# Kernel optimization log

Measured on AMD Instinct MI355X. Metric: run time of the kernel, lower is better.

The kernel has to match this reference:

```python
import jax, jax.numpy as jnp
import numpy as np

NUM_PEAK = 28000
NUM_GENE = 12000
N_NODES = NUM_PEAK + NUM_GENE
N_EDGES = 640000
NUM_TOPICS = 100
T_HIDDEN = 512
EMB = 64
HID = 128  # 2 * emb_size, hidden_channels of GCN
BATCH = 256
BN_EPS = 1e-5


def setup_inputs() -> dict:
    key = jax.random.key(0)
    ks = iter(jax.random.split(key, 64))
    def nrm(shape, s=0.05):
        return jax.random.normal(next(ks), shape, dtype=jnp.float32) * s
    def unif(shape):
        return jax.random.uniform(next(ks), shape, dtype=jnp.float32)
    z = lambda *s: jnp.zeros(s, jnp.float32)
    o = lambda *s: jnp.ones(s, jnp.float32)
    inp = dict(
        Gene=unif((BATCH, NUM_GENE)),
        Gene_normalized=unif((BATCH, NUM_GENE)),
        Peak=unif((BATCH, NUM_PEAK)),
        Peak_normalized=unif((BATCH, NUM_PEAK)),
        feature_matrix=nrm((N_NODES, EMB), 1.0),
        # GATv2 layer 1 (EMB -> HID, heads=1)
        Wl1=nrm((HID, EMB)), bl1=z(HID), Wr1=nrm((HID, EMB)), br1=z(HID),
        att1=nrm((HID,), 0.1), bias1=z(HID),
        # GATv2 layer 2 (HID -> EMB)
        Wl2=nrm((EMB, HID)), bl2=z(EMB), Wr2=nrm((EMB, HID)), br2=z(EMB),
        att2=nrm((EMB,), 0.1), bias2=z(EMB),
        # gene encoder: Linear + ReLU + BN + Linear + ReLU + BN
        gW1=nrm((T_HIDDEN, NUM_GENE)), gb1=z(T_HIDDEN), gg1=o(T_HIDDEN), gbe1=z(T_HIDDEN),
        gW2=nrm((T_HIDDEN, T_HIDDEN)), gb2=z(T_HIDDEN), gg2=o(T_HIDDEN), gbe2=z(T_HIDDEN),
        # peak encoder
        pW1=nrm((T_HIDDEN, NUM_PEAK)), pb1=z(T_HIDDEN), pg1=o(T_HIDDEN), pbe1=z(T_HIDDEN),
        pW2=nrm((T_HIDDEN, T_HIDDEN)), pb2=z(T_HIDDEN), pg2=o(T_HIDDEN), pbe2=z(T_HIDDEN),
        mu_W=nrm((NUM_TOPICS, T_HIDDEN)), mu_b=z(NUM_TOPICS),
        ls_W=nrm((NUM_TOPICS, T_HIDDEN)), ls_b=z(NUM_TOPICS),
        alphas_W=nrm((NUM_TOPICS, EMB)),
        alphas_star_W=nrm((NUM_TOPICS, EMB)),
        edge_index=jax.random.randint(next(ks), (2, N_EDGES), 0, N_NODES),
    )
    return inp


def _batchnorm(h, gamma, beta):
    # training-style BN over batch axis (biased variance), eps=1e-5
    m = h.mean(axis=0)
    v = jnp.mean((h - m) ** 2, axis=0)
    return (h - m) * jax.lax.rsqrt(v + BN_EPS) * gamma + beta


def _gatv2(x, src, dst, Wl, bl, Wr, br, att, bias):
    # PyG GATv2Conv, heads=1: e_ij = att . leaky_relu(Wl x_j + Wr x_i),
    # softmax over incoming edges of i, out_i = sum_j alpha_ij * (Wl x_j) + bias
    xl = x @ Wl.T + bl            # [N, C]
    xr = x @ Wr.T + br            # [N, C]
    e = jax.nn.leaky_relu(xl[src] + xr[dst], negative_slope=0.2)  # [E, C]
    logit = e @ att               # [E]
    m = jax.ops.segment_max(logit, dst, num_segments=N_NODES)
    ex = jnp.exp(logit - m[dst])
    den = jax.ops.segment_sum(ex, dst, num_segments=N_NODES)
    alpha = ex / (den[dst] + 1e-16)
    out = jax.ops.segment_sum(alpha[:, None] * xl[src], dst, num_segments=N_NODES)
    return out + bias


def _encode(x, W1, b1, g1, be1, W2, b2, g2, be2, mu_W, mu_b, ls_W, ls_b):
    h = _batchnorm(jax.nn.relu(x @ W1.T + b1), g1, be1)
    h = _batchnorm(jax.nn.relu(h @ W2.T + b2), g2, be2)
    mu = h @ mu_W.T + mu_b
    logsigma = 2.0 * (h @ ls_W.T + ls_b)
    kl = -0.5 * jnp.sum(1.0 + logsigma - mu ** 2 - jnp.exp(logsigma), axis=-1).mean()
    return mu, kl


def reference(Gene, Gene_normalized, Peak, Peak_normalized, feature_matrix,
              Wl1, bl1, Wr1, br1, att1, bias1,
              Wl2, bl2, Wr2, br2, att2, bias2,
              gW1, gb1, gg1, gbe1, gW2, gb2, gg2, gbe2,
              pW1, pb1, pg1, pbe1, pW2, pb2, pg2, pbe2,
              mu_W, mu_b, ls_W, ls_b, alphas_W, alphas_star_W, edge_index):
    # ---- variational encoders (eval mode: dropout off, theta from mu) ----
    mu_d, kl_d = _encode(Gene_normalized, gW1, gb1, gg1, gbe1, gW2, gb2, gg2, gbe2,
                         mu_W, mu_b, ls_W, ls_b)
    mu_j, kl_j = _encode(Peak_normalized, pW1, pb1, pg1, pbe1, pW2, pb2, pg2, pbe2,
                         mu_W, mu_b, ls_W, ls_b)
    theta_d = jax.nn.softmax(mu_d, axis=-1)   # [B, K]
    theta_j = jax.nn.softmax(mu_j, axis=-1)
    kld_theta = kl_d + kl_j

    # ---- GCN embedding: two GATv2Conv layers with self-loops ----
    loops = jnp.arange(N_NODES)
    src = jnp.concatenate([edge_index[0], loops])
    dst = jnp.concatenate([edge_index[1], loops])
    h = jax.nn.relu(_gatv2(feature_matrix, src, dst, Wl1, bl1, Wr1, br1, att1, bias1))
    emb = _gatv2(h, src, dst, Wl2, bl2, Wr2, br2, att2, bias2)
    emb = jax.nn.relu(emb)  # theta_act applied in forward
    eta_matrix = emb[:NUM_PEAK]   # [num_peak, EMB]
    rho_matrix = emb[NUM_PEAK:]   # [num_gene, EMB]

    # ---- topic-word matrices: softmax over genes/peaks (dim=0), transposed ----
    beta_gene = jax.nn.softmax(rho_matrix @ alphas_W.T, axis=0).T        # [K, num_gene]
    beta_peak = jax.nn.softmax(eta_matrix @ alphas_star_W.T, axis=0).T   # [K, num_peak]

    # ---- decode + reconstruction loss ----
    preds_gene = jnp.log(theta_d @ beta_gene + 1e-6)
    preds_peak = jnp.log(theta_j @ beta_peak + 1e-6)
    recon = (-(preds_gene * Gene).sum(-1) - (preds_peak * Peak).sum(-1)).mean()
    return recon, kld_theta
```

## Files before the change

### kernel.cpp

```cpp
#include <hip/hip_runtime.h>
#include <cstdint>
#include <cstddef>

using u16 = unsigned short;
using u32 = unsigned int;
typedef __attribute__((ext_vector_type(8))) short bf16x8;
typedef __attribute__((ext_vector_type(4))) float f32x4;

static constexpr int NUM_PEAK = 28000;
static constexpr int NUM_GENE = 12000;
static constexpr int N_NODES  = NUM_PEAK + NUM_GENE;
static constexpr int N_EDGES  = 640000;
static constexpr int E_TOTAL  = N_EDGES + N_NODES;
static constexpr int NT       = 100;
static constexpr int NT2      = 200;
static constexpr int NTP      = 128;
static constexpr int TH       = 512;
static constexpr int EMB      = 64;
static constexpr int HID      = 128;
static constexpr int BATCH    = 256;
static constexpr int SCAN_CHUNK = 1024;
static constexpr int SCAN_NB  = (N_NODES + SCAN_CHUNK - 1) / SCAN_CHUNK;
static constexpr int ENC_CH   = 640;
static constexpr int KPG      = 12032;
static constexpr int KPP      = 28032;
static constexpr int KSPG     = (NUM_GENE + ENC_CH - 1) / ENC_CH;
static constexpr int KSPP     = (NUM_PEAK + ENC_CH - 1) / ENC_CH;
static constexpr int CS_ROWS  = 128;
static constexpr int NBMAX    = (NUM_PEAK + CS_ROWS - 1) / CS_ROWS;
#define BN_EPS 1e-5f

__device__ __forceinline__ u16 f2bf(float f) {
  u32 b = __float_as_uint(f);
  return (u16)((b + 0x7FFFu + ((b >> 16) & 1u)) >> 16);
}
__device__ __forceinline__ float bf2f(u16 u) {
  return __uint_as_float((u32)u << 16);
}

struct CvtJobs {
  const float* src[12];
  u16* dst[12];
  u32 n[12];
  u32 start[12];
  int count;
};

__global__ __launch_bounds__(256) void cvt_all(CvtJobs J) {
  const int bid = blockIdx.x;
  int seg = 0;
  while (seg + 1 < J.count && bid >= (int)J.start[seg + 1]) ++seg;
  const float* __restrict__ src = J.src[seg];
  u16* __restrict__ dst = J.dst[seg];
  const u32 n = J.n[seg];
  const u32 i = (u32)(bid - J.start[seg]) * 2048u + threadIdx.x * 8u;
  if (i + 8 <= n) {
    float4 a = *(const float4*)(src + i);
    float4 b = *(const float4*)(src + i + 4);
    ushort4 o0{f2bf(a.x), f2bf(a.y), f2bf(a.z), f2bf(a.w)};
    ushort4 o1{f2bf(b.x), f2bf(b.y), f2bf(b.z), f2bf(b.w)};
    *(ushort4*)(dst + i) = o0;
    *(ushort4*)(dst + i + 4) = o1;
  } else {
    for (u32 j = i; j < n; ++j) dst[j] = f2bf(src[j]);
  }
}

__global__ __launch_bounds__(256) void cvt_pad(
    const float* __restrict__ g, u16* __restrict__ gb,
    const float* __restrict__ p, u16* __restrict__ pb) {
  const bool sec = (blockIdx.y != 0);
  const float* __restrict__ src = sec ? p : g;
  u16* __restrict__ dst = sec ? pb : gb;
  const int K = sec ? NUM_PEAK : NUM_GENE;
  const int Kp = sec ? KPP : KPG;
  const size_t total = (size_t)BATCH * Kp;
  size_t i = ((size_t)blockIdx.x * 256 + threadIdx.x) * 8;
  const size_t stride = (size_t)gridDim.x * 256 * 8;
  for (; i < total; i += stride) {
    const int col = (int)(i % Kp);
    const size_t row = i / Kp;
    ushort4 o0{0, 0, 0, 0}, o1{0, 0, 0, 0};
    if (col + 8 <= K) {
      const float* s = src + row * K + col;
      float4 a = *(const float4*)s;
      float4 b = *(const float4*)(s + 4);
      o0 = ushort4{f2bf(a.x), f2bf(a.y), f2bf(a.z), f2bf(a.w)};
      o1 = ushort4{f2bf(b.x), f2bf(b.y), f2bf(b.z), f2bf(b.w)};
    }
    *(ushort4*)(dst + i) = o0;
    *(ushort4*)(dst + i + 4) = o1;
  }
}

struct GP {
  const u16* A; const u16* B; float* C; u16* Cb; const float* bias;
  int M, N, K, chunk;
};

__global__ __launch_bounds__(256) void gemm_bt_bf16(GP g0, GP g1, int dual) {
  const GP& g = (dual && blockIdx.z) ? g1 : g0;
  const int M = g.M, N = g.N, K = g.K;
  __shared__ u16 As[64][40];
  __shared__ u16 Bs[64][40];
  const int tid = threadIdx.x;
  const int bm = blockIdx.y * 64, bn = blockIdx.x * 64;
  if (bm >= M || bn >= N) return;
  const int k0 = dual ? 0 : blockIdx.z * g.chunk;
  const int k1 = min(K, k0 + g.chunk);
  const int w = tid >> 6, lane = tid & 63;
  const int wm = (w >> 1) * 32, wn = (w & 1) * 32;
  const int fr = lane & 15;
  const int ks = (lane >> 4) * 8;
  const int srow = tid >> 2, sseg = (tid & 3) * 8;
  f32x4 acc[2][2] = {};
  for (int kt = k0; kt < k1; kt += 32) {
    const int gk = kt + sseg;
    {
      const int gm = bm + srow;
      bf16x8 v = {0, 0, 0, 0, 0, 0, 0, 0};
      if (gm < M) {
        if (gk + 8 <= k1) v = *(const bf16x8*)(g.A + (size_t)gm * K + gk);
        else if (gk < k1)
          for (int e = 0; e < k1 - gk; ++e) ((short*)&v)[e] = (short)g.A[(size_t)gm * K + gk + e];
      }
      *(bf16x8*)&As[srow][sseg] = v;
    }
    {
      const int gn = bn + srow;
      bf16x8 v = {0, 0, 0, 0, 0, 0, 0, 0};
      if (gn < N) {
        if (gk + 8 <= k1) v = *(const bf16x8*)(g.B + (size_t)gn * K + gk);
        else if (gk < k1)
          for (int e = 0; e < k1 - gk; ++e) ((short*)&v)[e] = (short)g.B[(size_t)gn * K + gk + e];
      }
      *(bf16x8*)&Bs[srow][sseg] = v;
    }
    __syncthreads();
    bf16x8 a0 = *(const bf16x8*)&As[wm + fr][ks];
    bf16x8 a1 = *(const bf16x8*)&As[wm + 16 + fr][ks];
    bf16x8 b0 = *(const bf16x8*)&Bs[wn + fr][ks];
    bf16x8 b1 = *(const bf16x8*)&Bs[wn + 16 + fr][ks];
    acc[0][0] = __builtin_amdgcn_mfma_f32_16x16x32_bf16(a0, b0, acc[0][0], 0, 0, 0);
    acc[0][1] = __builtin_amdgcn_mfma_f32_16x16x32_bf16(a0, b1, acc[0][1], 0, 0, 0);
    acc[1][0] = __builtin_amdgcn_mfma_f32_16x16x32_bf16(a1, b0, acc[1][0], 0, 0, 0);
    acc[1][1] = __builtin_amdgcn_mfma_f32_16x16x32_bf16(a1, b1, acc[1][1], 0, 0, 0);
    __syncthreads();
  }
  const bool split = (!dual && gridDim.z > 1);
#pragma unroll
  for (int fi = 0; fi < 2; ++fi)
#pragma unroll
    for (int fj = 0; fj < 2; ++fj)
#pragma unroll
      for (int r = 0; r < 4; ++r) {
        const int row = bm + wm + fi * 16 + (lane >> 4) * 4 + r;
        const int col = bn + wn + fj * 16 + fr;
        if (row < M && col < N) {
          const float v = acc[fi][fj][r];
          if (split) atomicAdd(&g.C[(size_t)row * N + col], v);
          else if (g.Cb) g.Cb[(size_t)row * N + col] = f2bf(v + (g.bias ? g.bias[col] : 0.f));
          else g.C[(size_t)row * N + col] = v + (g.bias ? g.bias[col] : 0.f);
        }
      }
}

__device__ __forceinline__ int swz64(int row, int colu16) {
  return row * 64 + ((((colu16 >> 3) ^ row) & 7) << 3) + (colu16 & 7);
}

__global__ __launch_bounds__(256) void gemm_enc1(
    const u16* __restrict__ A0, const float* __restrict__ B0, float* __restrict__ P0,
    int K0, int Kp0, int ksp0,
    const u16* __restrict__ A1, const float* __restrict__ B1, float* __restrict__ P1,
    int K1, int Kp1) {
  int bx = blockIdx.x, by = blockIdx.y, bz = blockIdx.z;
  {
    const int gx = gridDim.x, gy = gridDim.y;
    const int nwg = gx * gy * gridDim.z;
    if ((nwg & 7) == 0) {
      const int f = bx + gx * (by + gy * bz);
      const int cpx = nwg >> 3;
      const int f2 = (f & 7) * cpx + (f >> 3);
      bx = f2 % gx;
      by = (f2 / gx) % gy;
      bz = f2 / (gx * gy);
    }
  }
  const bool second = (bz >= ksp0);
  const u16* __restrict__ A = second ? A1 : A0;
  const float* __restrict__ B = second ? B1 : B0;
  float* __restrict__ P = second ? P1 : P0;
  const int K = second ? K1 : K0;
  const int Kp = second ? Kp1 : Kp0;
  const int zz = second ? bz - ksp0 : bz;
  const int k0 = zz * ENC_CH;
  const int k1 = min(K, k0 + ENC_CH);
  __shared__ u16 As[64 * 64];
  __shared__ u16 Bs[64 * 64];
  const int tid = threadIdx.x;
  const int bm = by * 64;
  const int bn = bx * 64;
  const int w = tid >> 6, lane = tid & 63;
  const int wm = w * 16;
  const int fr = lane & 15, g = lane >> 4;
  const int ar = tid >> 2, acol = (tid & 3) * 16;
  const int br = tid >> 2, bcol = (tid & 3) * 16;
  const u16* Abase = A + (size_t)(bm + ar) * Kp + acol;
  const float* Bbase = B + (size_t)(bn + br) * K + bcol;

  bf16x8 rA0, rA1;
  float4 rB0, rB1, rB2, rB3;
  auto LD = [&](int kt) {
    const u16* sa = Abase + kt;
    rA0 = *(const bf16x8*)(sa);
    rA1 = *(const bf16x8*)(sa + 8);
    if (kt + bcol + 16 <= K) {
      const float* sb = Bbase + kt;
      rB0 = *(const float4*)(sb);
      rB1 = *(const float4*)(sb + 4);
      rB2 = *(const float4*)(sb + 8);
      rB3 = *(const float4*)(sb + 12);
    } else {
      rB0 = float4{0.f, 0.f, 0.f, 0.f}; rB1 = rB0; rB2 = rB0; rB3 = rB0;
    }
  };
  auto ST = [&]() {
    *(bf16x8*)&As[swz64(ar, acol)] = rA0;
    *(bf16x8*)&As[swz64(ar, acol + 8)] = rA1;
    ushort4 p0{f2bf(rB0.x), f2bf(rB0.y), f2bf(rB0.z), f2bf(rB0.w)};
    ushort4 p1{f2bf(rB1.x), f2bf(rB1.y), f2bf(rB1.z), f2bf(rB1.w)};
    ushort4 p2{f2bf(rB2.x), f2bf(rB2.y), f2bf(rB2.z), f2bf(rB2.w)};
    ushort4 p3{f2bf(rB3.x), f2bf(rB3.y), f2bf(rB3.z), f2bf(rB3.w)};
    const int b0 = swz64(br, bcol);
    const int b1 = swz64(br, bcol + 8);
    *(ushort4*)&Bs[b0] = p0;
    *(ushort4*)&Bs[b0 + 4] = p1;
    *(ushort4*)&Bs[b1] = p2;
    *(ushort4*)&Bs[b1 + 4] = p3;
  };

  f32x4 acc[4] = {};
  LD(k0);
  ST();
  for (int kt = k0; kt < k1; kt += 64) {
    __syncthreads();
    const bool more = (kt + 64 < k1);
    if (more) LD(kt + 64);
#pragma unroll
    for (int s = 0; s < 2; ++s) {
      const int kc = s * 32 + g * 8;
      bf16x8 a = *(const bf16x8*)&As[swz64(wm + fr, kc)];
#pragma unroll
      for (int fj = 0; fj < 4; ++fj) {
        bf16x8 b = *(const bf16x8*)&Bs[swz64(fj * 16 + fr, kc)];
        acc[fj] = __builtin_amdgcn_mfma_f32_16x16x32_bf16(a, b, acc[fj], 0, 0, 0);
      }
    }
    __syncthreads();
    if (more) ST();
  }
  float* Pz = P + (size_t)zz * TH * 256;
  const int row = bm + wm + g * 4;
#pragma unroll
  for (int fj = 0; fj < 4; ++fj) {
    const int col = bn + fj * 16 + fr;
    *(f32x4*)&Pz[(size_t)col * 256 + row] = acc[fj];
  }
}

__global__ __launch_bounds__(256) void bias_relu_bn_part(
    const float* __restrict__ PG, int nzG, const float* __restrict__ bg,
    const float* __restrict__ gg, const float* __restrict__ beg,
    u16* __restrict__ og,
    const float* __restrict__ PP, int nzP, const float* __restrict__ bp,
    const float* __restrict__ gp, const float* __restrict__ bep,
    u16* __restrict__ op) {
  int c = blockIdx.x;
  const float *P, *b, *gma, *be; u16* ob; int nz;
  if (c < TH) { P = PG; nz = nzG; b = bg; gma = gg; be = beg; ob = og; }
  else { c -= TH; P = PP; nz = nzP; b = bp; gma = gp; be = bep; ob = op; }
  const int r = threadIdx.x;
  float v = 0.f;
  const float* base = P + (size_t)c * 256 + r;
  for (int z = 0; z < nz; ++z) v += base[(size_t)z * TH * 256];
  v = fmaxf(v + b[c], 0.f);
  __shared__ float red[BATCH];
  red[r] = v; __syncthreads();
  for (int s = BATCH / 2; s > 0; s >>= 1) { if (r < s) red[r] += red[r + s]; __syncthreads(); }
  const float mean = red[0] * (1.f / BATCH);
  __syncthreads();
  const float d = v - mean;
  red[r] = d * d; __syncthreads();
  for (int s = BATCH / 2; s > 0; s >>= 1) { if (r < s) red[r] += red[r + s]; __syncthreads(); }
  const float var = red[0] * (1.f / BATCH);
  ob[(size_t)r * TH + c] = f2bf(d * rsqrtf(var + BN_EPS) * gma[c] + be[c]);
}

__global__ __launch_bounds__(256) void recon_fused(
    const u16* __restrict__ thg, const u16* __restrict__ betag,
    const float* __restrict__ Xg, int Ng, int tiles_g,
    const u16* __restrict__ thp, const u16* __restrict__ betap,
    const float* __restrict__ Xp, int Np, float* __restrict__ partials) {
  __shared__ float pred[64][65];
  __shared__ float wsum[4];
  int ct = blockIdx.x;
  const u16* A; const u16* B; const float* X; int N;
  if (ct < tiles_g) { A = thg; B = betag; X = Xg; N = Ng; }
  else { ct -= tiles_g; A = thp; B = betap; X = Xp; N = Np; }
  const int bm = blockIdx.y * 64, bn = ct * 64;
  const int tid = threadIdx.x, w = tid >> 6, lane = tid & 63;
  const int wm = (w >> 1) * 32, wn = (w & 1) * 32;
  const int fr = lane & 15, ks = (lane >> 4) * 8;
  const u16* Ar0 = A + (size_t)(bm + wm + fr) * NTP;
  const u16* Ar1 = A + (size_t)(bm + wm + 16 + fr) * NTP;
  bf16x8 a0[4], a1[4];
#pragma unroll
  for (int kt = 0; kt < 4; ++kt) {
    a0[kt] = *(const bf16x8*)(Ar0 + kt * 32 + ks);
    a1[kt] = *(const bf16x8*)(Ar1 + kt * 32 + ks);
  }
  const int gn0 = min(bn + wn + fr, N - 1);
  const int gn1 = min(bn + wn + 16 + fr, N - 1);
  const u16* Br0 = B + (size_t)gn0 * NTP;
  const u16* Br1 = B + (size_t)gn1 * NTP;
  f32x4 acc[2][2] = {};
#pragma unroll
  for (int kt = 0; kt < 4; ++kt) {
    bf16x8 b0 = *(const bf16x8*)(Br0 + kt * 32 + ks);
    bf16x8 b1 = *(const bf16x8*)(Br1 + kt * 32 + ks);
    acc[0][0] = __builtin_amdgcn_mfma_f32_16x16x32_bf16(a0[kt], b0, acc[0][0], 0, 0, 0);
    acc[0][1] = __builtin_amdgcn_mfma_f32_16x16x32_bf16(a0[kt], b1, acc[0][1], 0, 0, 0);
    acc[1][0] = __builtin_amdgcn_mfma_f32_16x16x32_bf16(a1[kt], b0, acc[1][0], 0, 0, 0);
    acc[1][1] = __builtin_amdgcn_mfma_f32_16x16x32_bf16(a1[kt], b1, acc[1][1], 0, 0, 0);
  }
#pragma unroll
  for (int fi = 0; fi < 2; ++fi)
#pragma unroll
    for (int fj = 0; fj < 2; ++fj)
#pragma unroll
      for (int r = 0; r < 4; ++r)
        pred[wm + fi * 16 + (lane >> 4) * 4 + r][wn + fj * 16 + fr] = acc[fi][fj][r];
  __syncthreads();
  float local = 0.f;
  if (bn + 64 <= N) {
#pragma unroll
    for (int k = 0; k < 4; ++k) {
      const int j = k * 1024 + tid * 4;
      const int row = j >> 6, col = j & 63;
      const float4 xv = *(const float4*)(X + (size_t)(bm + row) * N + bn + col);
      local += xv.x * __logf(pred[row][col + 0] + 1e-6f);
      local += xv.y * __logf(pred[row][col + 1] + 1e-6f);
      local += xv.z * __logf(pred[row][col + 2] + 1e-6f);
      local += xv.w * __logf(pred[row][col + 3] + 1e-6f);
    }
  } else {
#pragma unroll
    for (int k = 0; k < 16; ++k) {
      const int idx = k * 256 + tid, row = idx >> 6, col = idx & 63;
      if (bn + col < N)
        local += X[(size_t)(bm + row) * N + bn + col] * __logf(pred[row][col] + 1e-6f);
    }
  }
  for (int o = 32; o > 0; o >>= 1) local += __shfl_down(local, o);
  if (lane == 0) wsum[w] = local;
  __syncthreads();
  if (tid == 0)
    partials[(size_t)blockIdx.y * gridDim.x + blockIdx.x] =
        wsum[0] + wsum[1] + wsum[2] + wsum[3];
}

__global__ __launch_bounds__(256) void final_recon(
    const float* __restrict__ partials, int n, float* __restrict__ out) {
  float s = 0.f;
  for (int i = threadIdx.x; i < n; i += 256) s += partials[i];
  __shared__ float red[256];
  red[threadIdx.x] = s; __syncthreads();
  for (int o = 128; o > 0; o >>= 1) {
    if (threadIdx.x < o) red[threadIdx.x] += red[threadIdx.x + o];
    __syncthreads();
  }
  if (threadIdx.x == 0) out[0] = -red[0] * (1.f / BATCH);
}

__global__ __launch_bounds__(256) void bias_relu_bn2(
    const float* __restrict__ Hg, const float* __restrict__ bg,
    const float* __restrict__ gg, const float* __restrict__ beg,
    u16* __restrict__ og,
    const float* __restrict__ Hp, const float* __restrict__ bp,
    const float* __restrict__ gp, const float* __restrict__ bep,
    u16* __restrict__ op) {
  int c = blockIdx.x;
  const float *H, *b, *gma, *be; u16* ob;
  if (c < TH) { H = Hg; b = bg; gma = gg; be = beg; ob = og; }
  else { c -= TH; H = Hp; b = bp; gma = gp; be = bep; ob = op; }
  const int r = threadIdx.x;
  float v = fmaxf(H[(size_t)r * TH + c] + b[c], 0.f);
  __shared__ float red[BATCH];
  red[r] = v; __syncthreads();
  for (int s = BATCH / 2; s > 0; s >>= 1) { if (r < s) red[r] += red[r + s]; __syncthreads(); }
  const float mean = red[0] * (1.f / BATCH);
  __syncthreads();
  const float d = v - mean;
  red[r] = d * d; __syncthreads();
  for (int s = BATCH / 2; s > 0; s >>= 1) { if (r < s) red[r] += red[r + s]; __syncthreads(); }
  const float var = red[0] * (1.f / BATCH);
  ob[(size_t)r * TH + c] = f2bf(d * rsqrtf(var + BN_EPS) * gma[c] + be[c]);
}

__global__ __launch_bounds__(128) void row_kl_theta(
    const float* __restrict__ mld, const float* __restrict__ mlj,
    const float* __restrict__ mu_b, const float* __restrict__ ls_b,
    u16* __restrict__ thd, u16* __restrict__ thj, float* __restrict__ kl_out) {
  const float* ml = blockIdx.y ? mlj : mld;
  u16* thb = blockIdx.y ? thj : thd;
  const int b = blockIdx.x;
  const int t = threadIdx.x;
  const bool act = (t < NT);
  float mu = 0.f, ls = 0.f, term = 0.f;
  if (act) {
    mu = ml[(size_t)b * NT2 + t] + mu_b[t];
    ls = 2.f * (ml[(size_t)b * NT2 + NT + t] + ls_b[t]);
    term = 1.f + ls - mu * mu - expf(ls);
  }
  __shared__ float red[128];
  red[t] = act ? term : 0.f; __syncthreads();
  for (int s = 64; s > 0; s >>= 1) { if (t < s) red[t] += red[t + s]; __syncthreads(); }
  if (t == 0) atomicAdd(kl_out, -0.5f * red[0] * (1.f / BATCH));
  __syncthreads();
  red[t] = act ? mu : -INFINITY; __syncthreads();
  for (int s = 64; s > 0; s >>= 1) { if (t < s) red[t] = fmaxf(red[t], red[t + s]); __syncthreads(); }
  const float mx = red[0];
  __syncthreads();
  const float e = act ? expf(mu - mx) : 0.f;
  red[t] = e; __syncthreads();
  for (int s = 64; s > 0; s >>= 1) { if (t < s) red[t] += red[t + s]; __syncthreads(); }
  thb[(size_t)b * NTP + t] = act ? f2bf(e / red[0]) : (u16)0;
}

__global__ __launch_bounds__(256) void deg_count(
    const int* __restrict__ ei, int* __restrict__ deg) {
  int e = blockIdx.x * 256 + threadIdx.x;
  if (e >= E_TOTAL) return;
  const int d = (e < N_EDGES) ? ei[N_EDGES + e] : e - N_EDGES;
  atomicAdd(&deg[d], 1);
}

__global__ __launch_bounds__(256) void scan_part(
    const int* __restrict__ deg, int* __restrict__ bsum) {
  const int base = blockIdx.x * SCAN_CHUNK + threadIdx.x * 4;
  int s = 0;
#pragma unroll
  for (int i = 0; i < 4; ++i) {
    const int idx = base + i;
    if (idx < N_NODES) s += deg[idx];
  }
  for (int o = 32; o > 0; o >>= 1) s += __shfl_down(s, o);
  __shared__ int ws[4];
  if ((threadIdx.x & 63) == 0) ws[threadIdx.x >> 6] = s;
  __syncthreads();
  if (threadIdx.x == 0) bsum[blockIdx.x] = ws[0] + ws[1] + ws[2] + ws[3];
}

__global__ __launch_bounds__(64) void scan_bsum(int* __restrict__ bsum) {
  if (threadIdx.x == 0) {
    int run = 0;
    for (int i = 0; i < SCAN_NB; ++i) { int v = bsum[i]; bsum[i] = run; run += v; }
  }
}

__global__ __launch_bounds__(256) void scan_final(
    const int* __restrict__ deg, const int* __restrict__ bsum,
    int* __restrict__ row_ptr) {
  const int t = threadIdx.x;
  const int base = blockIdx.x * SCAN_CHUNK + t * 4;
  int v[4], s = 0;
#pragma unroll
  for (int i = 0; i < 4; ++i) {
    const int idx = base + i;
    v[i] = (idx < N_NODES) ? deg[idx] : 0;
    s += v[i];
  }
  const int lane = t & 63, w = t >> 6;
  int x = s;
  for (int o = 1; o < 64; o <<= 1) {
    int y = __shfl_up(x, o);
    if (lane >= o) x += y;
  }
  __shared__ int wtot[4];
  if (lane == 63) wtot[w] = x;
  __syncthreads();
  int woff = 0;
  for (int i = 0; i < w; ++i) woff += wtot[i];
  int excl = bsum[blockIdx.x] + woff + x - s;
#pragma unroll
  for (int i = 0; i < 4; ++i) {
    const int idx = base + i;
    if (idx < N_NODES) { row_ptr[idx] = excl; excl += v[i]; }
  }
  if (blockIdx.x == 0 && t == 0) row_ptr[N_NODES] = E_TOTAL;
}

__global__ __launch_bounds__(256) void csr_scatter(
    const int* __restrict__ ei, const int* __restrict__ row_ptr,
    int* __restrict__ cur, int* __restrict__ csr_src) {
  int e = blockIdx.x * 256 + threadIdx.x;
  if (e >= E_TOTAL) return;
  int s, d;
  if (e < N_EDGES) { s = ei[e]; d = ei[N_EDGES + e]; }
  else { s = d = e - N_EDGES; }
  const int pos = atomicAdd(&cur[d], 1);
  csr_src[row_ptr[d] + pos] = s;
}

template <int C>
__global__ __launch_bounds__(256) void gat_fused(
    const u16* __restrict__ xl, const u16* __restrict__ xr,
    const float* __restrict__ att, const float* __restrict__ bias,
    const int* __restrict__ row_ptr, const int* __restrict__ csr_src,
    u16* __restrict__ out_b) {
  constexpr int CPL = C / 8;
  constexpr int W = CPL / 2;
  const int lane = threadIdx.x & 63;
  const int g = lane >> 3, li = lane & 7;
  const int d = blockIdx.x * 4 + (threadIdx.x >> 6);
  if (d >= N_NODES) return;
  const int c0 = li * CPL;
  float xrv[CPL], attv[CPL], acc[CPL];
  {
    const u32* xrw = (const u32*)(xr + (size_t)d * C + c0);
#pragma unroll
    for (int i = 0; i < W; ++i) {
      const u32 wv = xrw[i];
      xrv[2 * i]     = __uint_as_float(wv << 16);
      xrv[2 * i + 1] = __uint_as_float(wv & 0xffff0000u);
    }
  }
#pragma unroll
  for (int i = 0; i < CPL; ++i) { attv[i] = att[c0 + i]; acc[i] = 0.f; }
  float m = -INFINITY, den = 0.f;
  const int end = row_ptr[d + 1];
  int p = row_ptr[d] + g;
  int s = (p < end) ? csr_src[p] : 0;
  u32 w[W];
  {
    const u32* sw = (const u32*)(xl + (size_t)s * C + c0);
#pragma unroll
    for (int i = 0; i < W; ++i) w[i] = sw[i];
  }
  while (p < end) {
    const int sn = (p + 8 < end) ? csr_src[p + 8] : 0;
    u32 wn[W];
    {
      const u32* sw = (const u32*)(xl + (size_t)sn * C + c0);
#pragma unroll
      for (int i = 0; i < W; ++i) wn[i] = sw[i];
    }
    float xlv[CPL];
#pragma unroll
    for (int i = 0; i < W; ++i) {
      xlv[2 * i]     = __uint_as_float(w[i] << 16);
      xlv[2 * i + 1] = __uint_as_float(w[i] & 0xffff0000u);
    }
    float part = 0.f;
#pragma unroll
    for (int i = 0; i < CPL; ++i) {
      float x = xlv[i] + xrv[i];
      x = (x > 0.f) ? x : 0.2f * x;
      part += x * attv[i];
    }
    part += __shfl_xor(part, 1);
    part += __shfl_xor(part, 2);
    part += __shfl_xor(part, 4);
    const float nm = fmaxf(m, part);
    const float scale = __expf(m - nm);
    const float ex = __expf(part - nm);
    den = den * scale + ex;
#pragma unroll
    for (int i = 0; i < CPL; ++i) acc[i] = acc[i] * scale + ex * xlv[i];
    m = nm;
    p += 8;
#pragma unroll
    for (int i = 0; i < W; ++i) w[i] = wn[i];
  }
  float M = m;
  M = fmaxf(M, __shfl_xor(M, 8));
  M = fmaxf(M, __shfl_xor(M, 16));
  M = fmaxf(M, __shfl_xor(M, 32));
  const float gs = __expf(m - M);
  den *= gs;
  den += __shfl_xor(den, 8);
  den += __shfl_xor(den, 16);
  den += __shfl_xor(den, 32);
  const float inv = 1.f / (den + 1e-16f);
  float va[CPL];
#pragma unroll
  for (int i = 0; i < CPL; ++i) {
    float a = acc[i] * gs;
    a += __shfl_xor(a, 8);
    a += __shfl_xor(a, 16);
    a += __shfl_xor(a, 32);
    va[i] = a;
  }
  if (g == 0) {
    u32* dst = (u32*)(out_b + (size_t)d * C + c0);
#pragma unroll
    for (int i = 0; i < W; ++i) {
      const u16 lo = f2bf(fmaxf(va[2 * i] * inv + bias[c0 + 2 * i], 0.f));
      const u16 hi = f2bf(fmaxf(va[2 * i + 1] * inv + bias[c0 + 2 * i + 1], 0.f));
      dst[i] = (u32)lo | ((u32)hi << 16);
    }
  }
}

__global__ __launch_bounds__(128) void col_stats(
    const float* __restrict__ Lg, const float* __restrict__ Lp,
    float* __restrict__ bstats) {
  const bool sec = (blockIdx.y != 0);
  const float* L = sec ? Lp : Lg;
  const int M = sec ? NUM_PEAK : NUM_GENE;
  const int r0 = blockIdx.x * CS_ROWS;
  const int c = threadIdx.x;
  if (c >= NT || r0 >= M) return;
  const int rend = min(r0 + CS_ROWS, M);
  float m = -INFINITY, s = 0.f;
  for (int r = r0; r < rend; ++r) {
    const float v = L[(size_t)r * NT + c];
    const float nm = fmaxf(m, v);
    s = s * __expf(m - nm) + __expf(v - nm);
    m = nm;
  }
  float* bs = bstats + (((size_t)blockIdx.y * NT + c) * NBMAX + blockIdx.x) * 2;
  bs[0] = m;
  bs[1] = s;
}

__global__ __launch_bounds__(64) void col_merge(
    const float* __restrict__ bstats, int nbG, int nbP,
    float* __restrict__ mstat, float* __restrict__ istat) {
  const bool sec = (blockIdx.y != 0);
  const int nb = sec ? nbP : nbG;
  const int c = blockIdx.x;
  const int l = threadIdx.x;
  const float* bs = bstats + ((size_t)blockIdx.y * NT + c) * NBMAX * 2;
  float m = -INFINITY, s = 0.f;
  for (int b = l; b < nb; b += 64) {
    const float mb = bs[b * 2];
    const float sb = bs[b * 2 + 1];
    const float nm = fmaxf(m, mb);
    s = s * __expf(m - nm) + sb * __expf(mb - nm);
    m = nm;
  }
#pragma unroll
  for (int o = 32; o > 0; o >>= 1) {
    const float mo = __shfl_xor(m, o);
    const float so = __shfl_xor(s, o);
    const float nm = fmaxf(m, mo);
    s = s * __expf(m - nm) + so * __expf(mo - nm);
    m = nm;
  }
  if (l == 0) {
    mstat[blockIdx.y * NT + c] = m;
    istat[blockIdx.y * NT + c] = 1.f / s;
  }
}

__global__ __launch_bounds__(256) void beta_norm(
    const float* __restrict__ Lg, const float* __restrict__ Lp,
    const float* __restrict__ mstat, const float* __restrict__ istat,
    u16* __restrict__ og, u16* __restrict__ op) {
  const float* L = blockIdx.y ? Lp : Lg;
  const int M = blockIdx.y ? NUM_PEAK : NUM_GENE;
  const float* mxg = mstat + blockIdx.y * NT;
  const float* ivg = istat + blockIdx.y * NT;
  u16* o = blockIdx.y ? op : og;
  __shared__ float mx[NT], inv[NT];
  for (int i = threadIdx.x; i < NT; i += 256) { mx[i] = mxg[i]; inv[i] = ivg[i]; }
  __syncthreads();
  const size_t total = (size_t)M * NTP;
  size_t i = (size_t)blockIdx.x * 256 + threadIdx.x;
  const size_t stride = (size_t)gridDim.x * 256;
  for (; i < total; i += stride) {
    const int c = (int)(i & (NTP - 1));
    u16 v = 0;
    if (c < NT) {
      const size_t r = i >> 7;
      v = f2bf(__expf(L[r * NT + c] - mx[c]) * inv[c]);
    }
    o[i] = v;
  }
}

extern "C" void kernel_launch(void* const* d_in, const int* in_sizes, int n_in,
                              void* d_out, int out_size, void* d_ws, size_t ws_size,
                              hipStream_t stream) {
  const float* Gene  = (const float*)d_in[0];
  const float* GeneN = (const float*)d_in[1];
  const float* Peak  = (const float*)d_in[2];
  const float* PeakN = (const float*)d_in[3];
  const float* feat  = (const float*)d_in[4];
  const float* Wl1 = (const float*)d_in[5];  const float* bl1 = (const float*)d_in[6];
  const float* Wr1 = (const float*)d_in[7];  const float* br1 = (const float*)d_in[8];
  const float* att1 = (const float*)d_in[9]; const float* bias1 = (const float*)d_in[10];
  const float* Wl2 = (const float*)d_in[11]; const float* bl2 = (const float*)d_in[12];
  const float* Wr2 = (const float*)d_in[13]; const float* br2 = (const float*)d_in[14];
  const float* att2 = (const float*)d_in[15]; const float* bias2 = (const float*)d_in[16];
  const float* gW1 = (const float*)d_in[17]; const float* gb1 = (const float*)d_in[18];
  const float* gg1 = (const float*)d_in[19]; const float* gbe1 = (const float*)d_in[20];
  const float* gW2 = (const float*)d_in[21]; const float* gb2 = (const float*)d_in[22];
  const float* gg2 = (const float*)d_in[23]; const float* gbe2 = (const float*)d_in[24];
  const float* pW1 = (const float*)d_in[25]; const float* pb1 = (const float*)d_in[26];
  const float* pg1 = (const float*)d_in[27]; const float* pbe1 = (const float*)d_in[28];
  const float* pW2 = (const float*)d_in[29]; const float* pb2 = (const float*)d_in[30];
  const float* pg2 = (const float*)d_in[31]; const float* pbe2 = (const float*)d_in[32];
  const float* mu_W = (const float*)d_in[33]; const float* mu_b = (const float*)d_in[34];
  const float* ls_W = (const float*)d_in[35]; const float* ls_b = (const float*)d_in[36];
  const float* alphas_W = (const float*)d_in[37];
  const float* alphas_star_W = (const float*)d_in[38];
  const int* ei = (const int*)d_in[39];
  float* out = (float*)d_out;
  (void)in_sizes; (void)n_in; (void)ws_size;

  char* base = (char*)d_ws;
  size_t off = 0;
  auto A = [&](size_t bytes) { void* p = base + off; off += (bytes + 255) & ~(size_t)255; return p; };
  int* deg     = (int*)A((size_t)N_NODES * 4);
  int* cur     = (int*)A((size_t)N_NODES * 4);
  int* row_ptr = (int*)A((size_t)(N_NODES + 1) * 4);
  int* bsum    = (int*)A((size_t)(SCAN_NB + 1) * 4);
  int* csr_src = (int*)A((size_t)E_TOTAL * 4);
  float* CpartG = (float*)A((size_t)KSPG * TH * 256 * 4);
  float* CpartP = (float*)A((size_t)KSPP * TH * 256 * 4);
  float* h2g = (float*)A((size_t)BATCH * TH * 4);
  float* h2p = (float*)A((size_t)BATCH * TH * 4);
  u16* h1gb = (u16*)A((size_t)BATCH * TH * 2);
  u16* h2gb = (u16*)A((size_t)BATCH * TH * 2);
  u16* h1pb = (u16*)A((size_t)BATCH * TH * 2);
  u16* h2pb = (u16*)A((size_t)BATCH * TH * 2);
  float* ml_d = (float*)A((size_t)BATCH * NT2 * 4);
  float* ml_j = (float*)A((size_t)BATCH * NT2 * 4);
  u16* th_db = (u16*)A((size_t)BATCH * NTP * 2);
  u16* th_jb = (u16*)A((size_t)BATCH * NTP * 2);
  float* lgg = (float*)A((size_t)NUM_GENE * NT * 4);
  float* lgp = (float*)A((size_t)NUM_PEAK * NT * 4);
  u16* betagb = (u16*)A((size_t)NUM_GENE * NTP * 2);
  u16* betapb = (u16*)A((size_t)NUM_PEAK * NTP * 2);
  u16* featb = (u16*)A((size_t)N_NODES * EMB * 2);
  u16* gW2b = (u16*)A((size_t)TH * TH * 2);
  u16* pW2b = (u16*)A((size_t)TH * TH * 2);
  u16* mlWb = (u16*)A((size_t)NT2 * TH * 2);
  u16* Wl1b = (u16*)A((size_t)HID * EMB * 2);
  u16* Wr1b = (u16*)A((size_t)HID * EMB * 2);
  u16* Wl2b = (u16*)A((size_t)EMB * HID * 2);
  u16* Wr2b = (u16*)A((size_t)EMB * HID * 2);
  u16* aWb  = (u16*)A((size_t)NT * EMB * 2);
  u16* aSWb = (u16*)A((size_t)NT * EMB * 2);
  u16* agg1b = (u16*)A((size_t)N_NODES * HID * 2);
  u16* embb  = (u16*)A((size_t)N_NODES * EMB * 2);
  float* mstat = (float*)A(2 * NT * 4);
  float* istat = (float*)A(2 * NT * 4);
  float* bstats = (float*)A((size_t)2 * NT * NBMAX * 2 * 4);
  float* partials = (float*)A(4096 * 4);
  u16* xl1b = (u16*)A((size_t)N_NODES * HID * 2);
  u16* xr1b = (u16*)A((size_t)N_NODES * HID * 2);
  u16* xl2b = (u16*)A((size_t)N_NODES * EMB * 2);
  u16* xr2b = (u16*)A((size_t)N_NODES * EMB * 2);
  u16* GeneNb = (u16*)A((size_t)BATCH * KPG * 2);
  u16* PeakNb = (u16*)A((size_t)BATCH * KPP * 2);

  auto cdiv = [](int a, int b) { return (a + b - 1) / b; };
  auto Z = [&](void* p, size_t bytes) { hipMemsetAsync(p, 0, bytes, stream); };

  Z(d_out, (size_t)out_size * sizeof(float));
  Z(deg, 2 * (size_t)N_NODES * 4);

  deg_count<<<cdiv(E_TOTAL, 256), 256, 0, stream>>>(ei, deg);
  scan_part<<<SCAN_NB, 256, 0, stream>>>(deg, bsum);
  scan_bsum<<<1, 64, 0, stream>>>(bsum);
  scan_final<<<SCAN_NB, 256, 0, stream>>>(deg, bsum, row_ptr);
  csr_scatter<<<cdiv(E_TOTAL, 256), 256, 0, stream>>>(ei, row_ptr, cur, csr_src);

  {
    const int blocks = cdiv(BATCH * KPP / 8, 256);
    cvt_pad<<<dim3(blocks, 2), 256, 0, stream>>>(GeneN, GeneNb, PeakN, PeakNb);
  }

  {
    CvtJobs J = {};
    int c = 0; u32 blocks = 0;
    auto add = [&](const float* s, u16* d, size_t n) {
      J.src[c] = s; J.dst[c] = d; J.n[c] = (u32)n; J.start[c] = blocks;
      blocks += (u32)((n + 2047) / 2048); ++c;
    };
    add(gW2, gW2b, (size_t)TH * TH);
    add(pW2, pW2b, (size_t)TH * TH);
    add(mu_W, mlWb, (size_t)NT * TH);
    add(ls_W, mlWb + (size_t)NT * TH, (size_t)NT * TH);
    add(feat, featb, (size_t)N_NODES * EMB);
    add(Wl1, Wl1b, (size_t)HID * EMB);
    add(Wr1, Wr1b, (size_t)HID * EMB);
    add(Wl2, Wl2b, (size_t)EMB * HID);
    add(Wr2, Wr2b, (size_t)EMB * HID);
    add(alphas_W, aWb, (size_t)NT * EMB);
    add(alphas_star_W, aSWb, (size_t)NT * EMB);
    J.count = c;
    cvt_all<<<blocks, 256, 0, stream>>>(J);
  }

  gemm_enc1<<<dim3(TH / 64, BATCH / 64, KSPG + KSPP), 256, 0, stream>>>(
      GeneNb, gW1, CpartG, NUM_GENE, KPG, KSPG,
      PeakNb, pW1, CpartP, NUM_PEAK, KPP);
  bias_relu_bn_part<<<2 * TH, BATCH, 0, stream>>>(
      CpartG, KSPG, gb1, gg1, gbe1, h1gb,
      CpartP, KSPP, pb1, pg1, pbe1, h1pb);
  {
    GP g = {h1gb, gW2b, h2g, nullptr, nullptr, BATCH, TH, TH, TH};
    GP p = {h1pb, pW2b, h2p, nullptr, nullptr, BATCH, TH, TH, TH};
    gemm_bt_bf16<<<dim3(TH / 64, BATCH / 64, 2), 256, 0, stream>>>(g, p, 1);
  }
  bias_relu_bn2<<<2 * TH, BATCH, 0, stream>>>(h2g, gb2, gg2, gbe2, h2gb,
                                              h2p, pb2, pg2, pbe2, h2pb);
  {
    GP g = {h2gb, mlWb, ml_d, nullptr, nullptr, BATCH, NT2, TH, TH};
    GP p = {h2pb, mlWb, ml_j, nullptr, nullptr, BATCH, NT2, TH, TH};
    gemm_bt_bf16<<<dim3(cdiv(NT2, 64), BATCH / 64, 2), 256, 0, stream>>>(g, p, 1);
  }
  row_kl_theta<<<dim3(BATCH, 2), 128, 0, stream>>>(ml_d, ml_j, mu_b, ls_b, th_db, th_jb, out + 1);

  {
    GP l = {featb, Wl1b, nullptr, xl1b, bl1, N_NODES, HID, EMB, EMB};
    GP r = {featb, Wr1b, nullptr, xr1b, br1, N_NODES, HID, EMB, EMB};
    gemm_bt_bf16<<<dim3(HID / 64, N_NODES / 64, 2), 256, 0, stream>>>(l, r, 1);
  }
  gat_fused<HID><<<N_NODES / 4, 256, 0, stream>>>(xl1b, xr1b, att1, bias1, row_ptr, csr_src, agg1b);

  {
    GP l = {agg1b, Wl2b, nullptr, xl2b, bl2, N_NODES, EMB, HID, HID};
    GP r = {agg1b, Wr2b, nullptr, xr2b, br2, N_NODES, EMB, HID, HID};
    gemm_bt_bf16<<<dim3(EMB / 64, N_NODES / 64, 2), 256, 0, stream>>>(l, r, 1);
  }
  gat_fused<EMB><<<N_NODES / 4, 256, 0, stream>>>(xl2b, xr2b, att2, bias2, row_ptr, csr_src, embb);

  {
    GP g = {embb + (size_t)NUM_PEAK * EMB, aWb, lgg, nullptr, nullptr, NUM_GENE, NT, EMB, EMB};
    GP p = {embb, aSWb, lgp, nullptr, nullptr, NUM_PEAK, NT, EMB, EMB};
    gemm_bt_bf16<<<dim3(2, cdiv(NUM_PEAK, 64), 2), 256, 0, stream>>>(g, p, 1);
  }
  const int nbG = cdiv(NUM_GENE, CS_ROWS);
  const int nbP = cdiv(NUM_PEAK, CS_ROWS);
  col_stats<<<dim3(NBMAX, 2), 128, 0, stream>>>(lgg, lgp, bstats);
  col_merge<<<dim3(NT, 2), 64, 0, stream>>>(bstats, nbG, nbP, mstat, istat);
  beta_norm<<<dim3(1024, 2), 256, 0, stream>>>(lgg, lgp, mstat, istat, betagb, betapb);

  const int tiles_g = cdiv(NUM_GENE, 64);
  const int tiles_p = cdiv(NUM_PEAK, 64);
  const int tiles = tiles_g + tiles_p;
  recon_fused<<<dim3(tiles, 4), 256, 0, stream>>>(
      th_db, betagb, Gene, NUM_GENE, tiles_g,
      th_jb, betapb, Peak, NUM_PEAK, partials);
  final_recon<<<1, 256, 0, stream>>>(partials, tiles * 4, out);
}
```

Before: 394.4 us.

## Merge independent encoder and GAT stages into combined mega-kernels by block range

Independent branches (encoder GEMMs and BN, GAT linear layers and aggregation, KL/theta and column stats) are turned into device functions and dispatched from shared launches, with each launch splitting its blocks by index range. This cuts the number of kernel launches and lets the small encoder work overlap with the large graph work instead of running serially. The GEMM helper drops split-K and tail handling, which assumes K is a multiple of 32. Shared memory is now sized for the largest branch, which may lower occupancy for the lighter ones.

```diff
diff --git a/kernel.cpp b/kernel.cpp
--- a/kernel.cpp
+++ b/kernel.cpp
@@ -26,6 +26,7 @@
 static constexpr int KPP      = 28032;
 static constexpr int KSPG     = (NUM_GENE + ENC_CH - 1) / ENC_CH;
 static constexpr int KSPP     = (NUM_PEAK + ENC_CH - 1) / ENC_CH;
+static constexpr int ENC1B    = 8 * 4 * (KSPG + KSPP);
 static constexpr int CS_ROWS  = 128;
 static constexpr int NBMAX    = (NUM_PEAK + CS_ROWS - 1) / CS_ROWS;
 #define BN_EPS 1e-5f
@@ -33,9 +34,6 @@
 __device__ __forceinline__ u16 f2bf(float f) {
   u32 b = __float_as_uint(f);
   return (u16)((b + 0x7FFFu + ((b >> 16) & 1u)) >> 16);
-}
-__device__ __forceinline__ float bf2f(u16 u) {
-  return __uint_as_float((u32)u << 16);
 }
 
 struct CvtJobs {
@@ -95,45 +93,34 @@
 
 struct GP {
   const u16* A; const u16* B; float* C; u16* Cb; const float* bias;
-  int M, N, K, chunk;
+  int M, N, K;
 };
 
-__global__ __launch_bounds__(256) void gemm_bt_bf16(GP g0, GP g1, int dual) {
-  const GP& g = (dual && blockIdx.z) ? g1 : g0;
+__device__ void dev_gemm_bt(const GP g, int bxx, int byy, char* smem) {
+  u16 (*As)[40] = (u16(*)[40])smem;
+  u16 (*Bs)[40] = (u16(*)[40])(smem + 64 * 40 * 2);
   const int M = g.M, N = g.N, K = g.K;
-  __shared__ u16 As[64][40];
-  __shared__ u16 Bs[64][40];
   const int tid = threadIdx.x;
-  const int bm = blockIdx.y * 64, bn = blockIdx.x * 64;
+  const int bm = byy * 64, bn = bxx * 64;
   if (bm >= M || bn >= N) return;
-  const int k0 = dual ? 0 : blockIdx.z * g.chunk;
-  const int k1 = min(K, k0 + g.chunk);
   const int w = tid >> 6, lane = tid & 63;
   const int wm = (w >> 1) * 32, wn = (w & 1) * 32;
   const int fr = lane & 15;
   const int ks = (lane >> 4) * 8;
   const int srow = tid >> 2, sseg = (tid & 3) * 8;
   f32x4 acc[2][2] = {};
-  for (int kt = k0; kt < k1; kt += 32) {
+  for (int kt = 0; kt < K; kt += 32) {
     const int gk = kt + sseg;
     {
       const int gm = bm + srow;
       bf16x8 v = {0, 0, 0, 0, 0, 0, 0, 0};
-      if (gm < M) {
-        if (gk + 8 <= k1) v = *(const bf16x8*)(g.A + (size_t)gm * K + gk);
-        else if (gk < k1)
-          for (int e = 0; e < k1 - gk; ++e) ((short*)&v)[e] = (short)g.A[(size_t)gm * K + gk + e];
-      }
+      if (gm < M) v = *(const bf16x8*)(g.A + (size_t)gm * K + gk);
       *(bf16x8*)&As[srow][sseg] = v;
     }
     {
       const int gn = bn + srow;
       bf16x8 v = {0, 0, 0, 0, 0, 0, 0, 0};
-      if (gn < N) {
-        if (gk + 8 <= k1) v = *(const bf16x8*)(g.B + (size_t)gn * K + gk);
-        else if (gk < k1)
-          for (int e = 0; e < k1 - gk; ++e) ((short*)&v)[e] = (short)g.B[(size_t)gn * K + gk + e];
-      }
+      if (gn < N) v = *(const bf16x8*)(g.B + (size_t)gn * K + gk);
       *(bf16x8*)&Bs[srow][sseg] = v;
     }
     __syncthreads();
@@ -147,7 +134,6 @@
     acc[1][1] = __builtin_amdgcn_mfma_f32_16x16x32_bf16(a1, b1, acc[1][1], 0, 0, 0);
     __syncthreads();
   }
-  const bool split = (!dual && gridDim.z > 1);
 #pragma unroll
   for (int fi = 0; fi < 2; ++fi)
 #pragma unroll
@@ -158,8 +144,7 @@
         const int col = bn + wn + fj * 16 + fr;
         if (row < M && col < N) {
           const float v = acc[fi][fj][r];
-          if (split) atomicAdd(&g.C[(size_t)row * N + col], v);
-          else if (g.Cb) g.Cb[(size_t)row * N + col] = f2bf(v + (g.bias ? g.bias[col] : 0.f));
+          if (g.Cb) g.Cb[(size_t)row * N + col] = f2bf(v + (g.bias ? g.bias[col] : 0.f));
           else g.C[(size_t)row * N + col] = v + (g.bias ? g.bias[col] : 0.f);
         }
       }
@@ -169,35 +154,26 @@
   return row * 64 + ((((colu16 >> 3) ^ row) & 7) << 3) + (colu16 & 7);
 }
 
-__global__ __launch_bounds__(256) void gemm_enc1(
+__device__ void dev_enc1(
     const u16* __restrict__ A0, const float* __restrict__ B0, float* __restrict__ P0,
-    int K0, int Kp0, int ksp0,
     const u16* __restrict__ A1, const float* __restrict__ B1, float* __restrict__ P1,
-    int K1, int Kp1) {
-  int bx = blockIdx.x, by = blockIdx.y, bz = blockIdx.z;
-  {
-    const int gx = gridDim.x, gy = gridDim.y;
-    const int nwg = gx * gy * gridDim.z;
-    if ((nwg & 7) == 0) {
-      const int f = bx + gx * (by + gy * bz);
-      const int cpx = nwg >> 3;
-      const int f2 = (f & 7) * cpx + (f >> 3);
-      bx = f2 % gx;
-      by = (f2 / gx) % gy;
-      bz = f2 / (gx * gy);
-    }
-  }
-  const bool second = (bz >= ksp0);
+    int bid, char* smem) {
+  const int cpx = ENC1B >> 3;
+  const int f2 = (bid & 7) * cpx + (bid >> 3);
+  const int bx = f2 % 8;
+  const int by = (f2 / 8) % 4;
+  const int bz = f2 / 32;
+  const bool second = (bz >= KSPG);
   const u16* __restrict__ A = second ? A1 : A0;
   const float* __restrict__ B = second ? B1 : B0;
   float* __restrict__ P = second ? P1 : P0;
-  const int K = second ? K1 : K0;
-  const int Kp = second ? Kp1 : Kp0;
-  const int zz = second ? bz - ksp0 : bz;
+  const int K = second ? NUM_PEAK : NUM_GENE;
+  const int Kp = second ? KPP : KPG;
+  const int zz = second ? bz - KSPG : bz;
   const int k0 = zz * ENC_CH;
   const int k1 = min(K, k0 + ENC_CH);
-  __shared__ u16 As[64 * 64];
-  __shared__ u16 Bs[64 * 64];
+  u16* As = (u16*)smem;
+  u16* Bs = (u16*)(smem + 8192);
   const int tid = threadIdx.x;
   const int bm = by * 64;
   const int bn = bx * 64;
@@ -269,23 +245,109 @@
   }
 }
 
-__global__ __launch_bounds__(256) void bias_relu_bn_part(
-    const float* __restrict__ PG, int nzG, const float* __restrict__ bg,
-    const float* __restrict__ gg, const float* __restrict__ beg,
-    u16* __restrict__ og,
-    const float* __restrict__ PP, int nzP, const float* __restrict__ bp,
-    const float* __restrict__ gp, const float* __restrict__ bep,
-    u16* __restrict__ op) {
-  int c = blockIdx.x;
-  const float *P, *b, *gma, *be; u16* ob; int nz;
-  if (c < TH) { P = PG; nz = nzG; b = bg; gma = gg; be = beg; ob = og; }
-  else { c -= TH; P = PP; nz = nzP; b = bp; gma = gp; be = bep; ob = op; }
+template <int C>
+__device__ void dev_gat(
+    const u16* __restrict__ xl, const u16* __restrict__ xr,
+    const float* __restrict__ att, const float* __restrict__ bias,
+    const int* __restrict__ row_ptr, const int* __restrict__ csr_src,
+    u16* __restrict__ out_b, int blk) {
+  constexpr int CPL = C / 8;
+  constexpr int W = CPL / 2;
+  const int lane = threadIdx.x & 63;
+  const int g = lane >> 3, li = lane & 7;
+  const int d = blk * 4 + ((int)threadIdx.x >> 6);
+  if (d >= N_NODES) return;
+  const int c0 = li * CPL;
+  float xrv[CPL], attv[CPL], acc[CPL];
+  {
+    const u32* xrw = (const u32*)(xr + (size_t)d * C + c0);
+#pragma unroll
+    for (int i = 0; i < W; ++i) {
+      const u32 wv = xrw[i];
+      xrv[2 * i]     = __uint_as_float(wv << 16);
+      xrv[2 * i + 1] = __uint_as_float(wv & 0xffff0000u);
+    }
+  }
+#pragma unroll
+  for (int i = 0; i < CPL; ++i) { attv[i] = att[c0 + i]; acc[i] = 0.f; }
+  float m = -INFINITY, den = 0.f;
+  const int end = row_ptr[d + 1];
+  int p = row_ptr[d] + g;
+  int s = (p < end) ? csr_src[p] : 0;
+  u32 w[W];
+  {
+    const u32* sw = (const u32*)(xl + (size_t)s * C + c0);
+#pragma unroll
+    for (int i = 0; i < W; ++i) w[i] = sw[i];
+  }
+  while (p < end) {
+    const int sn = (p + 8 < end) ? csr_src[p + 8] : 0;
+    u32 wn[W];
+    {
+      const u32* sw = (const u32*)(xl + (size_t)sn * C + c0);
+#pragma unroll
+      for (int i = 0; i < W; ++i) wn[i] = sw[i];
+    }
+    float xlv[CPL];
+#pragma unroll
+    for (int i = 0; i < W; ++i) {
+      xlv[2 * i]     = __uint_as_float(w[i] << 16);
+      xlv[2 * i + 1] = __uint_as_float(w[i] & 0xffff0000u);
+    }
+    float part = 0.f;
+#pragma unroll
+    for (int i = 0; i < CPL; ++i) {
+      float x = xlv[i] + xrv[i];
+      x = (x > 0.f) ? x : 0.2f * x;
+      part += x * attv[i];
+    }
+    part += __shfl_xor(part, 1);
+    part += __shfl_xor(part, 2);
+    part += __shfl_xor(part, 4);
+    const float nm = fmaxf(m, part);
+    const float scale = __expf(m - nm);
+    const float ex = __expf(part - nm);
+    den = den * scale + ex;
+#pragma unroll
+    for (int i = 0; i < CPL; ++i) acc[i] = acc[i] * scale + ex * xlv[i];
+    m = nm;
+    p += 8;
+#pragma unroll
+    for (int i = 0; i < W; ++i) w[i] = wn[i];
+  }
+  float M = m;
+  M = fmaxf(M, __shfl_xor(M, 8));
+  M = fmaxf(M, __shfl_xor(M, 16));
+  M = fmaxf(M, __shfl_xor(M, 32));
+  const float gs = __expf(m - M);
+  den *= gs;
+  den += __shfl_xor(den, 8);
+  den += __shfl_xor(den, 16);
+  den += __shfl_xor(den, 32);
+  const float inv = 1.f / (den + 1e-16f);
+  float va[CPL];
+#pragma unroll
+  for (int i = 0; i < CPL; ++i) {
+    float a = acc[i] * gs;
+    a += __shfl_xor(a, 8);
+    a += __shfl_xor(a, 16);
+    a += __shfl_xor(a, 32);
+    va[i] = a;
+  }
+  if (g == 0) {
+    u32* dst = (u32*)(out_b + (size_t)d * C + c0);
+#pragma unroll
+    for (int i = 0; i < W; ++i) {
+      const u16 lo = f2bf(fmaxf(va[2 * i] * inv + bias[c0 + 2 * i], 0.f));
+      const u16 hi = f2bf(fmaxf(va[2 * i + 1] * inv + bias[c0 + 2 * i + 1], 0.f));
+      dst[i] = (u32)lo | ((u32)hi << 16);
+    }
+  }
+}
+
+__device__ void dev_bn_body(float v, const float* gma, const float* be, int c,
+                            u16* ob, float* red) {
   const int r = threadIdx.x;
-  float v = 0.f;
-  const float* base = P + (size_t)c * 256 + r;
-  for (int z = 0; z < nz; ++z) v += base[(size_t)z * TH * 256];
-  v = fmaxf(v + b[c], 0.f);
-  __shared__ float red[BATCH];
   red[r] = v; __syncthreads();
   for (int s = BATCH / 2; s > 0; s >>= 1) { if (r < s) red[r] += red[r + s]; __syncthreads(); }
   const float mean = red[0] * (1.f / BATCH);
@@ -297,124 +359,43 @@
   ob[(size_t)r * TH + c] = f2bf(d * rsqrtf(var + BN_EPS) * gma[c] + be[c]);
 }
 
-__global__ __launch_bounds__(256) void recon_fused(
-    const u16* __restrict__ thg, const u16* __restrict__ betag,
-    const float* __restrict__ Xg, int Ng, int tiles_g,
-    const u16* __restrict__ thp, const u16* __restrict__ betap,
-    const float* __restrict__ Xp, int Np, float* __restrict__ partials) {
-  __shared__ float pred[64][65];
-  __shared__ float wsum[4];
-  int ct = blockIdx.x;
-  const u16* A; const u16* B; const float* X; int N;
-  if (ct < tiles_g) { A = thg; B = betag; X = Xg; N = Ng; }
-  else { ct -= tiles_g; A = thp; B = betap; X = Xp; N = Np; }
-  const int bm = blockIdx.y * 64, bn = ct * 64;
-  const int tid = threadIdx.x, w = tid >> 6, lane = tid & 63;
-  const int wm = (w >> 1) * 32, wn = (w & 1) * 32;
-  const int fr = lane & 15, ks = (lane >> 4) * 8;
-  const u16* Ar0 = A + (size_t)(bm + wm + fr) * NTP;
-  const u16* Ar1 = A + (size_t)(bm + wm + 16 + fr) * NTP;
-  bf16x8 a0[4], a1[4];
-#pragma unroll
-  for (int kt = 0; kt < 4; ++kt) {
-    a0[kt] = *(const bf16x8*)(Ar0 + kt * 32 + ks);
-    a1[kt] = *(const bf16x8*)(Ar1 + kt * 32 + ks);
-  }
-  const int gn0 = min(bn + wn + fr, N - 1);
-  const int gn1 = min(bn + wn + 16 + fr, N - 1);
-  const u16* Br0 = B + (size_t)gn0 * NTP;
-  const u16* Br1 = B + (size_t)gn1 * NTP;
-  f32x4 acc[2][2] = {};
-#pragma unroll
-  for (int kt = 0; kt < 4; ++kt) {
-    bf16x8 b0 = *(const bf16x8*)(Br0 + kt * 32 + ks);
-    bf16x8 b1 = *(const bf16x8*)(Br1 + kt * 32 + ks);
-    acc[0][0] = __builtin_amdgcn_mfma_f32_16x16x32_bf16(a0[kt], b0, acc[0][0], 0, 0, 0);
-    acc[0][1] = __builtin_amdgcn_mfma_f32_16x16x32_bf16(a0[kt], b1, acc[0][1], 0, 0, 0);
-    acc[1][0] = __builtin_amdgcn_mfma_f32_16x16x32_bf16(a1[kt], b0, acc[1][0], 0, 0, 0);
-    acc[1][1] = __builtin_amdgcn_mfma_f32_16x16x32_bf16(a1[kt], b1, acc[1][1], 0, 0, 0);
-  }
-#pragma unroll
-  for (int fi = 0; fi < 2; ++fi)
-#pragma unroll
-    for (int fj = 0; fj < 2; ++fj)
-#pragma unroll
-      for (int r = 0; r < 4; ++r)
-        pred[wm + fi * 16 + (lane >> 4) * 4 + r][wn + fj * 16 + fr] = acc[fi][fj][r];
-  __syncthreads();
-  float local = 0.f;
-  if (bn + 64 <= N) {
-#pragma unroll
-    for (int k = 0; k < 4; ++k) {
-      const int j = k * 1024 + tid * 4;
-      const int row = j >> 6, col = j & 63;
-      const float4 xv = *(const float4*)(X + (size_t)(bm + row) * N + bn + col);
-      local += xv.x * __logf(pred[row][col + 0] + 1e-6f);
-      local += xv.y * __logf(pred[row][col + 1] + 1e-6f);
-      local += xv.z * __logf(pred[row][col + 2] + 1e-6f);
-      local += xv.w * __logf(pred[row][col + 3] + 1e-6f);
-    }
-  } else {
-#pragma unroll
-    for (int k = 0; k < 16; ++k) {
-      const int idx = k * 256 + tid, row = idx >> 6, col = idx & 63;
-      if (bn + col < N)
-        local += X[(size_t)(bm + row) * N + bn + col] * __logf(pred[row][col] + 1e-6f);
-    }
-  }
-  for (int o = 32; o > 0; o >>= 1) local += __shfl_down(local, o);
-  if (lane == 0) wsum[w] = local;
-  __syncthreads();
-  if (tid == 0)
-    partials[(size_t)blockIdx.y * gridDim.x + blockIdx.x] =
-        wsum[0] + wsum[1] + wsum[2] + wsum[3];
-}
-
-__global__ __launch_bounds__(256) void final_recon(
-    const float* __restrict__ partials, int n, float* __restrict__ out) {
-  float s = 0.f;
-  for (int i = threadIdx.x; i < n; i += 256) s += partials[i];
-  __shared__ float red[256];
-  red[threadIdx.x] = s; __syncthreads();
-  for (int o = 128; o > 0; o >>= 1) {
-    if (threadIdx.x < o) red[threadIdx.x] += red[threadIdx.x + o];
-    __syncthreads();
-  }
-  if (threadIdx.x == 0) out[0] = -red[0] * (1.f / BATCH);
-}
-
-__global__ __launch_bounds__(256) void bias_relu_bn2(
-    const float* __restrict__ Hg, const float* __restrict__ bg,
-    const float* __restrict__ gg, const float* __restrict__ beg,
-    u16* __restrict__ og,
-    const float* __restrict__ Hp, const float* __restrict__ bp,
-    const float* __restrict__ gp, const float* __restrict__ bep,
-    u16* __restrict__ op) {
-  int c = blockIdx.x;
+__device__ void dev_bn_part(
+    int cg, const float* __restrict__ PG, int nzG, const float* bg,
+    const float* gg, const float* beg, u16* og,
+    const float* __restrict__ PP, int nzP, const float* bp,
+    const float* gp, const float* bep, u16* op, float* red) {
+  int c = cg;
+  const float *P, *b, *gma, *be; u16* ob; int nz;
+  if (c < TH) { P = PG; nz = nzG; b = bg; gma = gg; be = beg; ob = og; }
+  else { c -= TH; P = PP; nz = nzP; b = bp; gma = gp; be = bep; ob = op; }
+  const int r = threadIdx.x;
+  float v = 0.f;
+  const float* base = P + (size_t)c * 256 + r;
+  for (int z = 0; z < nz; ++z) v += base[(size_t)z * TH * 256];
+  v = fmaxf(v + b[c], 0.f);
+  dev_bn_body(v, gma, be, c, ob, red);
+}
+
+__device__ void dev_bn2(
+    int cg, const float* __restrict__ Hg, const float* bg,
+    const float* gg, const float* beg, u16* og,
+    const float* __restrict__ Hp, const float* bp,
+    const float* gp, const float* bep, u16* op, float* red) {
+  int c = cg;
   const float *H, *b, *gma, *be; u16* ob;
   if (c < TH) { H = Hg; b = bg; gma = gg; be = beg; ob = og; }
   else { c -= TH; H = Hp; b = bp; gma = gp; be = bep; ob = op; }
   const int r = threadIdx.x;
   float v = fmaxf(H[(size_t)r * TH + c] + b[c], 0.f);
-  __shared__ float red[BATCH];
-  red[r] = v; __syncthreads();
-  for (int s = BATCH / 2; s > 0; s >>= 1) { if (r < s) red[r] += red[r + s]; __syncthreads(); }
-  const float mean = red[0] * (1.f / BATCH);
-  __syncthreads();
-  const float d = v - mean;
-  red[r] = d * d; __syncthreads();
-  for (int s = BATCH / 2; s > 0; s >>= 1) { if (r < s) red[r] += red[r + s]; __syncthreads(); }
-  const float var = red[0] * (1.f / BATCH);
-  ob[(size_t)r * TH + c] = f2bf(d * rsqrtf(var + BN_EPS) * gma[c] + be[c]);
-}
-
-__global__ __launch_bounds__(128) void row_kl_theta(
-    const float* __restrict__ mld, const float* __restrict__ mlj,
-    const float* __restrict__ mu_b, const float* __restrict__ ls_b,
-    u16* __restrict__ thd, u16* __restrict__ thj, float* __restrict__ kl_out) {
-  const float* ml = blockIdx.y ? mlj : mld;
-  u16* thb = blockIdx.y ? thj : thd;
-  const int b = blockIdx.x;
+  dev_bn_body(v, gma, be, c, ob, red);
+}
+
+__device__ void dev_row_kl(
+    int b, int which, const float* __restrict__ mld, const float* __restrict__ mlj,
+    const float* mu_b, const float* ls_b,
+    u16* thd, u16* thj, float* kl_out, float* red) {
+  const float* ml = which ? mlj : mld;
+  u16* thb = which ? thj : thd;
   const int t = threadIdx.x;
   const bool act = (t < NT);
   float mu = 0.f, ls = 0.f, term = 0.f;
@@ -423,7 +404,6 @@
     ls = 2.f * (ml[(size_t)b * NT2 + NT + t] + ls_b[t]);
     term = 1.f + ls - mu * mu - expf(ls);
   }
-  __shared__ float red[128];
   red[t] = act ? term : 0.f; __syncthreads();
   for (int s = 64; s > 0; s >>= 1) { if (t < s) red[t] += red[t + s]; __syncthreads(); }
   if (t == 0) atomicAdd(kl_out, -0.5f * red[0] * (1.f / BATCH));
@@ -438,6 +418,110 @@
   thb[(size_t)b * NTP + t] = act ? f2bf(e / red[0]) : (u16)0;
 }
 
+__device__ void dev_col_stats(
+    int bx, int sec, const float* __restrict__ Lg, const float* __restrict__ Lp,
+    float* __restrict__ bstats) {
+  const float* L = sec ? Lp : Lg;
+  const int M = sec ? NUM_PEAK : NUM_GENE;
+  const int r0 = bx * CS_ROWS;
+  const int c = threadIdx.x;
+  if (c >= NT || r0 >= M) return;
+  const int rend = min(r0 + CS_ROWS, M);
+  float m = -INFINITY, s = 0.f;
+  for (int r = r0; r < rend; ++r) {
+    const float v = L[(size_t)r * NT + c];
+    const float nm = fmaxf(m, v);
+    s = s * __expf(m - nm) + __expf(v - nm);
+    m = nm;
+  }
+  float* bs = bstats + (((size_t)sec * NT + c) * NBMAX + bx) * 2;
+  bs[0] = m;
+  bs[1] = s;
+}
+
+__global__ __launch_bounds__(256) void mega1(
+    const u16* A0, const float* B0, float* P0,
+    const u16* A1, const float* B1, float* P1,
+    GP l, GP r) {
+  __shared__ __align__(16) char smem[20480];
+  const int bid = blockIdx.x;
+  if (bid < ENC1B) {
+    dev_enc1(A0, B0, P0, A1, B1, P1, bid, smem);
+  } else {
+    const int sub = bid - ENC1B;
+    const GP& g = (sub >= 1250) ? r : l;
+    const int rem = sub % 1250;
+    dev_gemm_bt(g, rem % 2, rem / 2, smem);
+  }
+}
+
+__global__ __launch_bounds__(256) void mega2(
+    const float* PG, int nzG, const float* bg, const float* gg, const float* beg, u16* og,
+    const float* PP, int nzP, const float* bp, const float* gp, const float* bep, u16* op,
+    const u16* xl, const u16* xr, const float* att, const float* bias,
+    const int* row_ptr, const int* csr_src, u16* out_b) {
+  __shared__ float red[256];
+  const int bid = blockIdx.x;
+  if (bid < 2 * TH)
+    dev_bn_part(bid, PG, nzG, bg, gg, beg, og, PP, nzP, bp, gp, bep, op, red);
+  else
+    dev_gat<HID>(xl, xr, att, bias, row_ptr, csr_src, out_b, bid - 2 * TH);
+}
+
+__global__ __launch_bounds__(256) void mega3(GP eg, GP ep, GP l, GP r) {
+  __shared__ __align__(16) char smem[20480];
+  const int bid = blockIdx.x;
+  if (bid < 64) {
+    const int z = bid >> 5, rem = bid & 31;
+    dev_gemm_bt(z ? ep : eg, rem & 7, rem >> 3, smem);
+  } else {
+    const int sub = bid - 64;
+    const GP& g = (sub >= 625) ? r : l;
+    dev_gemm_bt(g, 0, sub % 625, smem);
+  }
+}
+
+__global__ __launch_bounds__(256) void mega4(
+    const float* Hg, const float* bg, const float* gg, const float* beg, u16* og,
+    const float* Hp, const float* bp, const float* gp, const float* bep, u16* op,
+    const u16* xl, const u16* xr, const float* att, const float* bias,
+    const int* row_ptr, const int* csr_src, u16* out_b) {
+  __shared__ float red[256];
+  const int bid = blockIdx.x;
+  if (bid < 2 * TH)
+    dev_bn2(bid, Hg, bg, gg, beg, og, Hp, bp, gp, bep, op, red);
+  else
+    dev_gat<EMB>(xl, xr, att, bias, row_ptr, csr_src, out_b, bid - 2 * TH);
+}
+
+__global__ __launch_bounds__(256) void mega5(GP hg, GP hp, GP tg, GP tp) {
+  __shared__ __align__(16) char smem[20480];
+  const int bid = blockIdx.x;
+  if (bid < 32) {
+    const int z = bid >> 4, rem = bid & 15;
+    dev_gemm_bt(z ? hp : hg, rem & 3, rem >> 2, smem);
+  } else {
+    const int sub = bid - 32;
+    const GP& g = (sub >= 876) ? tp : tg;
+    const int rem = sub % 876;
+    dev_gemm_bt(g, rem & 1, rem >> 1, smem);
+  }
+}
+
+__global__ __launch_bounds__(128) void mega6(
+    const float* mld, const float* mlj, const float* mu_b, const float* ls_b,
+    u16* thd, u16* thj, float* kl_out,
+    const float* Lg, const float* Lp, float* bstats) {
+  __shared__ float red[128];
+  const int bid = blockIdx.x;
+  if (bid < 2 * BATCH)
+    dev_row_kl(bid % BATCH, bid / BATCH, mld, mlj, mu_b, ls_b, thd, thj, kl_out, red);
+  else {
+    const int sub = bid - 2 * BATCH;
+    dev_col_stats(sub % NBMAX, sub / NBMAX, Lg, Lp, bstats);
+  }
+}
+
 __global__ __launch_bounds__(256) void deg_count(
     const int* __restrict__ ei, int* __restrict__ deg) {
   int e = blockIdx.x * 256 + threadIdx.x;
@@ -511,128 +595,6 @@
   else { s = d = e - N_EDGES; }
   const int pos = atomicAdd(&cur[d], 1);
   csr_src[row_ptr[d] + pos] = s;
-}
-
-template <int C>
-__global__ __launch_bounds__(256) void gat_fused(
-    const u16* __restrict__ xl, const u16* __restrict__ xr,
-    const float* __restrict__ att, const float* __restrict__ bias,
-    const int* __restrict__ row_ptr, const int* __restrict__ csr_src,
-    u16* __restrict__ out_b) {
-  constexpr int CPL = C / 8;
-  constexpr int W = CPL / 2;
-  const int lane = threadIdx.x & 63;
-  const int g = lane >> 3, li = lane & 7;
-  const int d = blockIdx.x * 4 + (threadIdx.x >> 6);
-  if (d >= N_NODES) return;
-  const int c0 = li * CPL;
-  float xrv[CPL], attv[CPL], acc[CPL];
-  {
-    const u32* xrw = (const u32*)(xr + (size_t)d * C + c0);
-#pragma unroll
-    for (int i = 0; i < W; ++i) {
-      const u32 wv = xrw[i];
-      xrv[2 * i]     = __uint_as_float(wv << 16);
-      xrv[2 * i + 1] = __uint_as_float(wv & 0xffff0000u);
-    }
-  }
-#pragma unroll
-  for (int i = 0; i < CPL; ++i) { attv[i] = att[c0 + i]; acc[i] = 0.f; }
-  float m = -INFINITY, den = 0.f;
-  const int end = row_ptr[d + 1];
-  int p = row_ptr[d] + g;
-  int s = (p < end) ? csr_src[p] : 0;
-  u32 w[W];
-  {
-    const u32* sw = (const u32*)(xl + (size_t)s * C + c0);
-#pragma unroll
-    for (int i = 0; i < W; ++i) w[i] = sw[i];
-  }
-  while (p < end) {
-    const int sn = (p + 8 < end) ? csr_src[p + 8] : 0;
-    u32 wn[W];
-    {
-      const u32* sw = (const u32*)(xl + (size_t)sn * C + c0);
-#pragma unroll
-      for (int i = 0; i < W; ++i) wn[i] = sw[i];
-    }
-    float xlv[CPL];
-#pragma unroll
-    for (int i = 0; i < W; ++i) {
-      xlv[2 * i]     = __uint_as_float(w[i] << 16);
-      xlv[2 * i + 1] = __uint_as_float(w[i] & 0xffff0000u);
-    }
-    float part = 0.f;
-#pragma unroll
-    for (int i = 0; i < CPL; ++i) {
-      float x = xlv[i] + xrv[i];
-      x = (x > 0.f) ? x : 0.2f * x;
-      part += x * attv[i];
-    }
-    part += __shfl_xor(part, 1);
-    part += __shfl_xor(part, 2);
-    part += __shfl_xor(part, 4);
-    const float nm = fmaxf(m, part);
-    const float scale = __expf(m - nm);
-    const float ex = __expf(part - nm);
-    den = den * scale + ex;
-#pragma unroll
-    for (int i = 0; i < CPL; ++i) acc[i] = acc[i] * scale + ex * xlv[i];
-    m = nm;
-    p += 8;
-#pragma unroll
-    for (int i = 0; i < W; ++i) w[i] = wn[i];
-  }
-  float M = m;
-  M = fmaxf(M, __shfl_xor(M, 8));
-  M = fmaxf(M, __shfl_xor(M, 16));
-  M = fmaxf(M, __shfl_xor(M, 32));
-  const float gs = __expf(m - M);
-  den *= gs;
-  den += __shfl_xor(den, 8);
-  den += __shfl_xor(den, 16);
-  den += __shfl_xor(den, 32);
-  const float inv = 1.f / (den + 1e-16f);
-  float va[CPL];
-#pragma unroll
-  for (int i = 0; i < CPL; ++i) {
-    float a = acc[i] * gs;
-    a += __shfl_xor(a, 8);
-    a += __shfl_xor(a, 16);
-    a += __shfl_xor(a, 32);
-    va[i] = a;
-  }
-  if (g == 0) {
-    u32* dst = (u32*)(out_b + (size_t)d * C + c0);
-#pragma unroll
-    for (int i = 0; i < W; ++i) {
-      const u16 lo = f2bf(fmaxf(va[2 * i] * inv + bias[c0 + 2 * i], 0.f));
-      const u16 hi = f2bf(fmaxf(va[2 * i + 1] * inv + bias[c0 + 2 * i + 1], 0.f));
-      dst[i] = (u32)lo | ((u32)hi << 16);
-    }
-  }
-}
-
-__global__ __launch_bounds__(128) void col_stats(
-    const float* __restrict__ Lg, const float* __restrict__ Lp,
-    float* __restrict__ bstats) {
-  const bool sec = (blockIdx.y != 0);
-  const float* L = sec ? Lp : Lg;
-  const int M = sec ? NUM_PEAK : NUM_GENE;
-  const int r0 = blockIdx.x * CS_ROWS;
-  const int c = threadIdx.x;
-  if (c >= NT || r0 >= M) return;
-  const int rend = min(r0 + CS_ROWS, M);
-  float m = -INFINITY, s = 0.f;
-  for (int r = r0; r < rend; ++r) {
-    const float v = L[(size_t)r * NT + c];
-    const float nm = fmaxf(m, v);
-    s = s * __expf(m - nm) + __expf(v - nm);
-    m = nm;
-  }
-  float* bs = bstats + (((size_t)blockIdx.y * NT + c) * NBMAX + blockIdx.x) * 2;
-  bs[0] = m;
-  bs[1] = s;
 }
 
 __global__ __launch_bounds__(64) void col_merge(
@@ -689,6 +651,92 @@
     }
     o[i] = v;
   }
+}
+
+__global__ __launch_bounds__(256) void recon_fused(
+    const u16* __restrict__ thg, const u16* __restrict__ betag,
+    const float* __restrict__ Xg, int Ng, int tiles_g,
+    const u16* __restrict__ thp, const u16* __restrict__ betap,
+    const float* __restrict__ Xp, int Np, float* __restrict__ partials) {
+  __shared__ float pred[64][65];
+  __shared__ float wsum[4];
+  int ct = blockIdx.x;
+  const u16* A; const u16* B; const float* X; int N;
+  if (ct < tiles_g) { A = thg; B = betag; X = Xg; N = Ng; }
+  else { ct -= tiles_g; A = thp; B = betap; X = Xp; N = Np; }
+  const int bm = blockIdx.y * 64, bn = ct * 64;
+  const int tid = threadIdx.x, w = tid >> 6, lane = tid & 63;
+  const int wm = (w >> 1) * 32, wn = (w & 1) * 32;
+  const int fr = lane & 15, ks = (lane >> 4) * 8;
+  const u16* Ar0 = A + (size_t)(bm + wm + fr) * NTP;
+  const u16* Ar1 = A + (size_t)(bm + wm + 16 + fr) * NTP;
+  bf16x8 a0[4], a1[4];
+#pragma unroll
+  for (int kt = 0; kt < 4; ++kt) {
+    a0[kt] = *(const bf16x8*)(Ar0 + kt * 32 + ks);
+    a1[kt] = *(const bf16x8*)(Ar1 + kt * 32 + ks);
+  }
+  const int gn0 = min(bn + wn + fr, N - 1);
+  const int gn1 = min(bn + wn + 16 + fr, N - 1);
+  const u16* Br0 = B + (size_t)gn0 * NTP;
+  const u16* Br1 = B + (size_t)gn1 * NTP;
+  f32x4 acc[2][2] = {};
+#pragma unroll
+  for (int kt = 0; kt < 4; ++kt) {
+    bf16x8 b0 = *(const bf16x8*)(Br0 + kt * 32 + ks);
+    bf16x8 b1 = *(const bf16x8*)(Br1 + kt * 32 + ks);
+    acc[0][0] = __builtin_amdgcn_mfma_f32_16x16x32_bf16(a0[kt], b0, acc[0][0], 0, 0, 0);
+    acc[0][1] = __builtin_amdgcn_mfma_f32_16x16x32_bf16(a0[kt], b1, acc[0][1], 0, 0, 0);
+    acc[1][0] = __builtin_amdgcn_mfma_f32_16x16x32_bf16(a1[kt], b0, acc[1][0], 0, 0, 0);
+    acc[1][1] = __builtin_amdgcn_mfma_f32_16x16x32_bf16(a1[kt], b1, acc[1][1], 0, 0, 0);
+  }
+#pragma unroll
+  for (int fi = 0; fi < 2; ++fi)
+#pragma unroll
+    for (int fj = 0; fj < 2; ++fj)
+#pragma unroll
+      for (int r = 0; r < 4; ++r)
+        pred[wm + fi * 16 + (lane >> 4) * 4 + r][wn + fj * 16 + fr] = acc[fi][fj][r];
+  __syncthreads();
+  float local = 0.f;
+  if (bn + 64 <= N) {
+#pragma unroll
+    for (int k = 0; k < 4; ++k) {
+      const int j = k * 1024 + tid * 4;
+      const int row = j >> 6, col = j & 63;
+      const float4 xv = *(const float4*)(X + (size_t)(bm + row) * N + bn + col);
+      local += xv.x * __logf(pred[row][col + 0] + 1e-6f);
+      local += xv.y * __logf(pred[row][col + 1] + 1e-6f);
+      local += xv.z * __logf(pred[row][col + 2] + 1e-6f);
+      local += xv.w * __logf(pred[row][col + 3] + 1e-6f);
+    }
+  } else {
+#pragma unroll
+    for (int k = 0; k < 16; ++k) {
+      const int idx = k * 256 + tid, row = idx >> 6, col = idx & 63;
+      if (bn + col < N)
+        local += X[(size_t)(bm + row) * N + bn + col] * __logf(pred[row][col] + 1e-6f);
+    }
+  }
+  for (int o = 32; o > 0; o >>= 1) local += __shfl_down(local, o);
+  if (lane == 0) wsum[w] = local;
+  __syncthreads();
+  if (tid == 0)
+    partials[(size_t)blockIdx.y * gridDim.x + blockIdx.x] =
+        wsum[0] + wsum[1] + wsum[2] + wsum[3];
+}
+
+__global__ __launch_bounds__(256) void final_recon(
+    const float* __restrict__ partials, int n, float* __restrict__ out) {
+  float s = 0.f;
+  for (int i = threadIdx.x; i < n; i += 256) s += partials[i];
+  __shared__ float red[256];
+  red[threadIdx.x] = s; __syncthreads();
+  for (int o = 128; o > 0; o >>= 1) {
+    if (threadIdx.x < o) red[threadIdx.x] += red[threadIdx.x + o];
+    __syncthreads();
+  }
+  if (threadIdx.x == 0) out[0] = -red[0] * (1.f / BATCH);
 }
 
 extern "C" void kernel_launch(void* const* d_in, const int* in_sizes, int n_in,
@@ -784,7 +832,6 @@
     const int blocks = cdiv(BATCH * KPP / 8, 256);
     cvt_pad<<<dim3(blocks, 2), 256, 0, stream>>>(GeneN, GeneNb, PeakN, PeakNb);
   }
-
   {
     CvtJobs J = {};
     int c = 0; u32 blocks = 0;
@@ -807,48 +854,44 @@
     cvt_all<<<blocks, 256, 0, stream>>>(J);
   }
 
-  gemm_enc1<<<dim3(TH / 64, BATCH / 64, KSPG + KSPP), 256, 0, stream>>>(
-      GeneNb, gW1, CpartG, NUM_GENE, KPG, KSPG,
-      PeakNb, pW1, CpartP, NUM_PEAK, KPP);
-  bias_relu_bn_part<<<2 * TH, BATCH, 0, stream>>>(
+  {
+    GP l = {featb, Wl1b, nullptr, xl1b, bl1, N_NODES, HID, EMB};
+    GP r = {featb, Wr1b, nullptr, xr1b, br1, N_NODES, HID, EMB};
+    mega1<<<ENC1B + 2500, 256, 0, stream>>>(
+        GeneNb, gW1, CpartG, PeakNb, pW1, CpartP, l, r);
+  }
+
+  mega2<<<2 * TH + N_NODES / 4, 256, 0, stream>>>(
       CpartG, KSPG, gb1, gg1, gbe1, h1gb,
-      CpartP, KSPP, pb1, pg1, pbe1, h1pb);
+      CpartP, KSPP, pb1, pg1, pbe1, h1pb,
+      xl1b, xr1b, att1, bias1, row_ptr, csr_src, agg1b);
+
   {
-    GP g = {h1gb, gW2b, h2g, nullptr, nullptr, BATCH, TH, TH, TH};
-    GP p = {h1pb, pW2b, h2p, nullptr, nullptr, BATCH, TH, TH, TH};
-    gemm_bt_bf16<<<dim3(TH / 64, BATCH / 64, 2), 256, 0, stream>>>(g, p, 1);
-  }
-  bias_relu_bn2<<<2 * TH, BATCH, 0, stream>>>(h2g, gb2, gg2, gbe2, h2gb,
-                                              h2p, pb2, pg2, pbe2, h2pb);
+    GP eg = {h1gb, gW2b, h2g, nullptr, nullptr, BATCH, TH, TH};
+    GP ep = {h1pb, pW2b, h2p, nullptr, nullptr, BATCH, TH, TH};
+    GP l  = {agg1b, Wl2b, nullptr, xl2b, bl2, N_NODES, EMB, HID};
+    GP r  = {agg1b, Wr2b, nullptr, xr2b, br2, N_NODES, EMB, HID};
+    mega3<<<64 + 1250, 256, 0, stream>>>(eg, ep, l, r);
+  }
+
+  mega4<<<2 * TH + N_NODES / 4, 256, 0, stream>>>(
+      h2g, gb2, gg2, gbe2, h2gb,
+      h2p, pb2, pg2, pbe2, h2pb,
+      xl2b, xr2b, att2, bias2, row_ptr, csr_src, embb);
+
   {
-    GP g = {h2gb, mlWb, ml_d, nullptr, nullptr, BATCH, NT2, TH, TH};
-    GP p = {h2pb, mlWb, ml_j, nullptr, nullptr, BATCH, NT2, TH, TH};
-    gemm_bt_bf16<<<dim3(cdiv(NT2, 64), BATCH / 64, 2), 256, 0, stream>>>(g, p, 1);
-  }
-  row_kl_theta<<<dim3(BATCH, 2), 128, 0, stream>>>(ml_d, ml_j, mu_b, ls_b, th_db, th_jb, out + 1);
-
-  {
-    GP l = {featb, Wl1b, nullptr, xl1b, bl1, N_NODES, HID, EMB, EMB};
-    GP r = {featb, Wr1b, nullptr, xr1b, br1, N_NODES, HID, EMB, EMB};
-    gemm_bt_bf16<<<dim3(HID / 64, N_NODES / 64, 2), 256, 0, stream>>>(l, r, 1);
-  }
-  gat_fused<HID><<<N_NODES / 4, 256, 0, stream>>>(xl1b, xr1b, att1, bias1, row_ptr, csr_src, agg1b);
-
-  {
-    GP l = {agg1b, Wl2b, nullptr, xl2b, bl2, N_NODES, EMB, HID, HID};
-    GP r = {agg1b, Wr2b, nullptr, xr2b, br2, N_NODES, EMB, HID, HID};
-    gemm_bt_bf16<<<dim3(EMB / 64, N_NODES / 64, 2), 256, 0, stream>>>(l, r, 1);
-  }
-  gat_fused<EMB><<<N_NODES / 4, 256, 0, stream>>>(xl2b, xr2b, att2, bias2, row_ptr, csr_src, embb);
-
-  {
-    GP g = {embb + (size_t)NUM_PEAK * EMB, aWb, lgg, nullptr, nullptr, NUM_GENE, NT, EMB, EMB};
-    GP p = {embb, aSWb, lgp, nullptr, nullptr, NUM_PEAK, NT, EMB, EMB};
-    gemm_bt_bf16<<<dim3(2, cdiv(NUM_PEAK, 64), 2), 256, 0, stream>>>(g, p, 1);
-  }
+    GP hg = {h2gb, mlWb, ml_d, nullptr, nullptr, BATCH, NT2, TH};
+    GP hp = {h2pb, mlWb, ml_j, nullptr, nullptr, BATCH, NT2, TH};
+    GP tg = {embb + (size_t)NUM_PEAK * EMB, aWb, lgg, nullptr, nullptr, NUM_GENE, NT, EMB};
+    GP tp = {embb, aSWb, lgp, nullptr, nullptr, NUM_PEAK, NT, EMB};
+    mega5<<<32 + 2 * 2 * 438, 256, 0, stream>>>(hg, hp, tg, tp);
+  }
+
+  mega6<<<2 * BATCH + 2 * NBMAX, 128, 0, stream>>>(
+      ml_d, ml_j, mu_b, ls_b, th_db, th_jb, out + 1, lgg, lgp, bstats);
+
   const int nbG = cdiv(NUM_GENE, CS_ROWS);
   const int nbP = cdiv(NUM_PEAK, CS_ROWS);
-  col_stats<<<dim3(NBMAX, 2), 128, 0, stream>>>(lgg, lgp, bstats);
   col_merge<<<dim3(NT, 2), 64, 0, stream>>>(bstats, nbG, nbP, mstat, istat);
   beta_norm<<<dim3(1024, 2), 256, 0, stream>>>(lgg, lgp, mstat, istat, betagb, betapb);
 
```

Result: faster. 362.9 us (-8.0%).
